# Performance work log

Measured on AMD Instinct MI355X. Metric: run time of the kernel, lower is better.

## Reference

```python
import jax, jax.numpy as jnp
import numpy as np
from jax import lax

GROUPS = 32
EPS = 1e-5
N_STEPS = 8   # fixed-step stand-in for adaptive implicit_adams
N_CORR = 2    # trapezoidal (Adams-Moulton) corrector iterations


def group_norm(x, gamma, beta):
    B, C, H, W = x.shape
    xg = x.reshape(B, GROUPS, C // GROUPS, H, W)
    mean = xg.mean(axis=(2, 3, 4), keepdims=True)
    var = xg.var(axis=(2, 3, 4), keepdims=True)
    xg = (xg - mean) * lax.rsqrt(var + EPS)
    return xg.reshape(B, C, H, W) * gamma[None, :, None, None] + beta[None, :, None, None]


def batch_norm1d(x, gamma, beta):  # training-mode batch stats, x: [B,C,L]
    mean = x.mean(axis=(0, 2), keepdims=True)
    var = x.var(axis=(0, 2), keepdims=True)
    return (x - mean) * lax.rsqrt(var + EPS) * gamma[None, :, None] + beta[None, :, None]


def conv1d(x, w, b):  # x [B,Cin,L], w [Cout,Cin,3], pad=1
    y = lax.conv_general_dilated(x, w, (1,), [(1, 1)], dimension_numbers=('NCH', 'OIH', 'NCH'))
    return y + b[None, :, None]


def concat_conv2d(t, x, w, b):  # x [B,C,H,W], w [C, C+1, 3,3], pad=1
    tt = jnp.full_like(x[:, :1], t)
    ttx = jnp.concatenate([tt, x], axis=1)
    y = lax.conv_general_dilated(ttx, w, (1, 1), [(1, 1), (1, 1)], dimension_numbers=('NCHW', 'OIHW', 'NCHW'))
    return y + b[None, :, None, None]


def make_odefunc(cw1, cb1, gn1_g, gn1_b, gn2_g, gn2_b, cw2, cb2, gn3_g, gn3_b):
    def f(t, x):
        out = jax.nn.relu(group_norm(x, gn1_g, gn1_b))
        out = concat_conv2d(t, out, cw1, cb1)
        out = jax.nn.elu(group_norm(out, gn2_g, gn2_b))
        out = concat_conv2d(t, out, cw2, cb2)
        return group_norm(out, gn3_g, gn3_b)
    return f


def ode_integrate(f, y0):
    h = 1.0 / N_STEPS

    def step(y, i):
        t = i.astype(y.dtype) * h
        f0 = f(t, y)
        y1 = y + h * f0  # explicit predictor
        for _ in range(N_CORR):  # implicit (trapezoidal AM) corrector
            y1 = y + 0.5 * h * (f0 + f(t + h, y1))
        return y1, None

    yT, _ = lax.scan(step, y0, jnp.arange(N_STEPS))
    return yT


def setup_inputs() -> dict:
    key = jax.random.key(0)
    ks = jax.random.split(key, 8)
    B, L, C = 16, 4096, 256
    inp = {
        'x': jax.random.normal(ks[0], (B, 4, 1, L), dtype=jnp.float32),
        'w1': jax.random.normal(ks[1], (64, 4, 3), dtype=jnp.float32) * 0.1,
        'b1': jnp.zeros((64,), jnp.float32),
        'bn1_g': jnp.ones((64,), jnp.float32), 'bn1_b': jnp.zeros((64,), jnp.float32),
        'w2': jax.random.normal(ks[2], (256, 64, 3), dtype=jnp.float32) * 0.05,
        'b2': jnp.zeros((256,), jnp.float32),
        'bn2_g': jnp.ones((256,), jnp.float32), 'bn2_b': jnp.zeros((256,), jnp.float32),
        'cw1': jax.random.normal(ks[3], (C, C + 1, 3, 3), dtype=jnp.float32) * 0.02,
        'cb1': jnp.zeros((C,), jnp.float32),
        'gn1_g': jnp.ones((C,), jnp.float32), 'gn1_b': jnp.zeros((C,), jnp.float32),
        'gn2_g': jnp.ones((C,), jnp.float32), 'gn2_b': jnp.zeros((C,), jnp.float32),
        'cw2': jax.random.normal(ks[4], (C, C + 1, 3, 3), dtype=jnp.float32) * 0.02,
        'cb2': jnp.zeros((C,), jnp.float32),
        'gn3_g': jnp.ones((C,), jnp.float32), 'gn3_b': jnp.zeros((C,), jnp.float32),
    }
    return inp


def reference(x, w1, b1, bn1_g, bn1_b, w2, b2, bn2_g, bn2_b,
              cw1, cb1, gn1_g, gn1_b, gn2_g, gn2_b, cw2, cb2, gn3_g, gn3_b):
    h = x[:, :, 0, :]                       # squeeze(2) -> [B,4,L]
    h = jax.nn.relu(batch_norm1d(conv1d(h, w1, b1), bn1_g, bn1_b))
    h = jnp.tanh(batch_norm1d(conv1d(h, w2, b2), bn2_g, bn2_b))
    y0 = h[:, :, None, :]                   # unsqueeze(2) -> [B,256,1,L]
    f = make_odefunc(cw1, cb1, gn1_g, gn1_b, gn2_g, gn2_b, cw2, cb2, gn3_g, gn3_b)
    return ode_integrate(f, y0)
```

## Files before the change

kernel.cpp:

```cpp
#include <hip/hip_runtime.h>
#include <math.h>

#define L4 4096

typedef short bf16x8 __attribute__((ext_vector_type(8)));
typedef float f32x4 __attribute__((ext_vector_type(4)));

__device__ __forceinline__ unsigned short f2bf(float f) {
  unsigned u = __builtin_bit_cast(unsigned, f);
  return (unsigned short)((u + 0x7FFFu + ((u >> 16) & 1u)) >> 16);
}
__device__ __forceinline__ float bf2f(unsigned short h) {
  unsigned u = ((unsigned)h) << 16;
  return __builtin_bit_cast(float, u);
}
__device__ __forceinline__ unsigned pk2(float lo, float hi) {
  unsigned d;
  asm("v_cvt_pk_bf16_f32 %0, %1, %2" : "=v"(d) : "v"(lo), "v"(hi));
  return d;
}
__device__ __forceinline__ float fast_tanh(float x) {
  float e = __expf(2.f * x);
  return 1.f - 2.f * __builtin_amdgcn_rcpf(e + 1.f);
}

__global__ __launch_bounds__(256) void pack_big(const float* __restrict__ cw,
                                                unsigned short* __restrict__ Apack,
                                                float* __restrict__ Tpack) {
  int gid = blockIdx.x * 256 + threadIdx.x;
  if (gid < 768) {
    int o = gid & 255, tap = gid >> 8;
    Tpack[tap * 256 + o] = cw[((size_t)o * 257) * 9 + 3 + tap];
  }
  if (gid >= 24 * 16 * 64) return;
  int ks = gid >> 10;
  int frow = (gid >> 6) & 15;
  int lane = gid & 63;
  int o = frow * 16 + (lane & 15);
  int tap = ks >> 3;
  int ib = ((ks & 7) << 5) + ((lane >> 4) << 3);
#pragma unroll
  for (int e = 0; e < 8; e++) {
    int i = ib + e;
    Apack[(size_t)gid * 8 + e] = f2bf(cw[((size_t)o * 257 + (i + 1)) * 9 + 3 + tap]);
  }
}

__global__ __launch_bounds__(256) void pack_stem(const float* __restrict__ w2,
                                                 unsigned short* __restrict__ Apack) {
  int gid = blockIdx.x * 256 + threadIdx.x;
  if (gid >= 6 * 16 * 64) return;
  int ks = gid >> 10;
  int frow = (gid >> 6) & 15;
  int lane = gid & 63;
  int o = frow * 16 + (lane & 15);
  int tap = ks >> 1;
  int ib = ((ks & 1) << 5) + ((lane >> 4) << 3);
#pragma unroll
  for (int e = 0; e < 8; e++) {
    int i = ib + e;
    Apack[(size_t)gid * 8 + e] = f2bf(w2[((size_t)o * 64 + i) * 3 + tap]);
  }
}

__global__ __launch_bounds__(256) void conv1_kernel(const float* __restrict__ x,
                                                    const float* __restrict__ w,
                                                    const float* __restrict__ bias,
                                                    unsigned short* __restrict__ out) {
  int idx = blockIdx.x * 256 + threadIdx.x;
  int l = idx & 4095;
  int c = (idx >> 12) & 63;
  int b = idx >> 18;
  const float* xb = x + (size_t)b * 4 * L4;
  const float* wc = w + c * 12;
  float acc = bias[c];
#pragma unroll
  for (int i = 0; i < 4; i++) {
    float x0 = (l > 0) ? xb[i * L4 + l - 1] : 0.f;
    float x1 = xb[i * L4 + l];
    float x2 = (l < 4095) ? xb[i * L4 + l + 1] : 0.f;
    acc += wc[i * 3] * x0 + wc[i * 3 + 1] * x1 + wc[i * 3 + 2] * x2;
  }
  out[idx] = f2bf(acc);
}

__global__ __launch_bounds__(256) void stats_bf16_kernel(const unsigned short* __restrict__ in,
                                                         float* __restrict__ stats,
                                                         int unit_stride, int nrow,
                                                         int row_stride, int rowlen,
                                                         float inv_n) {
  int u = blockIdx.x;
  const unsigned short* base = in + (size_t)u * unit_stride;
  float s = 0.f, s2 = 0.f;
  for (int r = 0; r < nrow; r++) {
    const unsigned short* rowp = base + (size_t)r * row_stride;
    for (int j = threadIdx.x * 4; j < rowlen; j += 256 * 4) {
      ushort4 v = *(const ushort4*)(rowp + j);
      float va = bf2f(v.x), vb = bf2f(v.y), vc = bf2f(v.z), vd = bf2f(v.w);
      s += va + vb + vc + vd;
      s2 += va * va + vb * vb + vc * vc + vd * vd;
    }
  }
  __shared__ float sh[512];
  sh[threadIdx.x] = s;
  sh[256 + threadIdx.x] = s2;
  __syncthreads();
  for (int off = 128; off > 0; off >>= 1) {
    if (threadIdx.x < off) {
      sh[threadIdx.x] += sh[threadIdx.x + off];
      sh[256 + threadIdx.x] += sh[256 + threadIdx.x + off];
    }
    __syncthreads();
  }
  if (threadIdx.x == 0) {
    float m = sh[0] * inv_n;
    float var = sh[256] * inv_n - m * m;
    stats[u * 2] = m;
    stats[u * 2 + 1] = rsqrtf(var + 1e-5f);
  }
}

__global__ __launch_bounds__(256) void act_transpose64(const unsigned short* __restrict__ inv,
                                                       const float* __restrict__ stats,
                                                       const float* __restrict__ gamma,
                                                       const float* __restrict__ beta,
                                                       unsigned short* __restrict__ Xt) {
  constexpr int C = 64;
  __shared__ unsigned short tile[64 * C];
  int bidx = blockIdx.x;
  int b = bidx >> 6;
  int lt = bidx & 63;
  int l0 = lt << 6;
  int t = threadIdx.x;
  int lanel = t & 63;
  int cq = t >> 6;
  for (int cp = 0; cp < C / 4; cp++) {
    int c = cp * 4 + cq;
    float m = stats[2 * c], rs = stats[2 * c + 1];
    float ga = gamma[c] * rs, be = beta[c] - m * ga;
    size_t gidx = ((size_t)b * C + c) * 4096 + l0 + lanel;
    float v = bf2f(inv[gidx]);
    float a = v * ga + be;
    float r = fmaxf(a, 0.f);
    int sw = (lanel & 15) << 2;
    tile[lanel * C + (c ^ sw)] = f2bf(r);
  }
  __syncthreads();
  constexpr int CH = C / 4;
  constexpr int RPP = 256 / CH;
  for (int p = 0; p < 64 / RPP; p++) {
    int r = p * RPP + t / CH;
    int ch = t % CH;
    int sw = (r & 15) << 2;
    ushort4 v = *(const ushort4*)&tile[r * C + ((ch * 4) ^ sw)];
    *(ushort4*)&Xt[((size_t)b * 4098 + 1 + l0 + r) * C + ch * 4] = v;
  }
  if (lt == 0) {
    if (t < C / 4) *(ushort4*)&Xt[((size_t)b * 4098 + 0) * C + t * 4] = make_ushort4(0, 0, 0, 0);
  } else if (lt == 63) {
    if (t < C / 4) *(ushort4*)&Xt[((size_t)b * 4098 + 4097) * C + t * 4] = make_ushort4(0, 0, 0, 0);
  }
}

template <int NKS, int KLG, int CIN, int NORM, int ACT, int NCH, bool INBF, bool TCH, int OUT>
__global__ __launch_bounds__(512, 4) void gemm_T(const void* __restrict__ Bsrc,
                                                 const unsigned short* __restrict__ Apack,
                                                 const float* __restrict__ Pin,
                                                 const float* __restrict__ gng,
                                                 const float* __restrict__ gnb,
                                                 const float* __restrict__ Tpack,
                                                 const float* __restrict__ bias,
                                                 float tval,
                                                 void* __restrict__ outv,
                                                 float* __restrict__ Pout) {
  constexpr int CPR = CIN / 8;
  constexpr int CPRLG = (CIN == 256) ? 5 : 3;
  constexpr int ROWS = 66;
  constexpr int RPI = 512 >> CPRLG;
  constexpr int TOT = ROWS * CPR;
  constexpr int NIT = (TOT + 511) / 512;
  __shared__ unsigned short bsm[ROWS * CIN];
  __shared__ float gsm[32][2];
  __shared__ float ebias[256];
  __shared__ float psh[32][2];

  int tid = threadIdx.x;
  int lane = tid & 63;
  int wv = tid >> 6;
  int b = blockIdx.x >> 6;
  int lt = blockIdx.x & 63;
  int l_base = lt << 6;
  int wo0 = wv << 5;
  int col = lane & 15;
  int grp = lane >> 4;

  int pl = tid & (CPR - 1);
  int row0s = tid >> CPRLG;
  int gch = pl ^ (row0s & 7);
  uint4 hA[NIT];
  uint4 hB[NIT];
#pragma unroll
  for (int it = 0; it < NIT; it++) {
    hA[it] = make_uint4(0, 0, 0, 0);
    if (NORM && !INBF) hB[it] = make_uint4(0, 0, 0, 0);
    int chunk = it * 512 + tid;
    if (chunk < TOT) {
      int row = row0s + it * RPI;
      if (NORM) {
        int gl = l_base - 1 + row;
        if (gl >= 0 && gl < 4096) {
          size_t base = ((size_t)b * 4096 + gl) * CIN + gch * 8;
          if (INBF) {
            hA[it] = *(const uint4*)((const unsigned short*)Bsrc + base);
          } else {
            hA[it] = *(const uint4*)((const float*)Bsrc + base);
            hB[it] = *(const uint4*)((const float*)Bsrc + base + 4);
          }
        }
      } else {
        hA[it] = *(const uint4*)((const unsigned short*)Bsrc +
                                 ((size_t)b * 4098 + l_base + row) * CIN + gch * 8);
      }
    }
  }

  if (NORM) {
    int g = tid >> 4, j0 = tid & 15;
    const float* Pg = Pin + ((size_t)b * 32 + g) * 128;
    float s = 0.f, s2 = 0.f;
    for (int j = j0; j < NCH; j += 16) { s += Pg[j * 2]; s2 += Pg[j * 2 + 1]; }
#pragma unroll
    for (int off = 8; off; off >>= 1) { s += __shfl_down(s, off, 16); s2 += __shfl_down(s2, off, 16); }
    if (j0 == 0) {
      float m = s * (1.f / 32768.f);
      float var = s2 * (1.f / 32768.f) - m * m;
      gsm[g][0] = m;
      gsm[g][1] = rsqrtf(var + 1e-5f);
    }
  }
  if (tid < 256) {
    float e = bias[tid];
    if (TCH) e += tval * (Tpack[tid] + Tpack[256 + tid] + Tpack[512 + tid]);
    ebias[tid] = e;
  }
  if (OUT == 0 && tid >= 256 && tid < 288) { psh[tid - 256][0] = 0.f; psh[tid - 256][1] = 0.f; }
  __syncthreads();

  {
    float ga0 = 1.f, ga1 = 1.f, ga2 = 1.f, ga3 = 1.f, ga4 = 1.f, ga5 = 1.f, ga6 = 1.f, ga7 = 1.f;
    float be0 = 0.f, be1 = 0.f, be2 = 0.f, be3 = 0.f, be4 = 0.f, be5 = 0.f, be6 = 0.f, be7 = 0.f;
    if (NORM) {
      float m = gsm[gch][0], rs = gsm[gch][1];
      float4 g0 = *(const float4*)&gng[gch * 8];
      float4 g1 = *(const float4*)&gng[gch * 8 + 4];
      float4 b0 = *(const float4*)&gnb[gch * 8];
      float4 b1 = *(const float4*)&gnb[gch * 8 + 4];
      ga0 = g0.x * rs; ga1 = g0.y * rs; ga2 = g0.z * rs; ga3 = g0.w * rs;
      ga4 = g1.x * rs; ga5 = g1.y * rs; ga6 = g1.z * rs; ga7 = g1.w * rs;
      be0 = b0.x - m * ga0; be1 = b0.y - m * ga1; be2 = b0.z - m * ga2; be3 = b0.w - m * ga3;
      be4 = b1.x - m * ga4; be5 = b1.y - m * ga5; be6 = b1.z - m * ga6; be7 = b1.w - m * ga7;
    }
#define ACTF(a) ((ACT == 0) ? fmaxf((a), 0.f) : ((a) > 0.f ? (a) : __expf(a) - 1.f))
#pragma unroll
    for (int it = 0; it < NIT; it++) {
      int chunk = it * 512 + tid;
      if (chunk < TOT) {
        int row = row0s + it * RPI;
        uint4 w4;
        if (NORM) {
          int gl = l_base - 1 + row;
          if (gl >= 0 && gl < 4096) {
            float v0, v1, v2, v3, v4, v5, v6, v7;
            if (INBF) {
              v0 = bf2f((unsigned short)(hA[it].x & 0xFFFF)); v1 = bf2f((unsigned short)(hA[it].x >> 16));
              v2 = bf2f((unsigned short)(hA[it].y & 0xFFFF)); v3 = bf2f((unsigned short)(hA[it].y >> 16));
              v4 = bf2f((unsigned short)(hA[it].z & 0xFFFF)); v5 = bf2f((unsigned short)(hA[it].z >> 16));
              v6 = bf2f((unsigned short)(hA[it].w & 0xFFFF)); v7 = bf2f((unsigned short)(hA[it].w >> 16));
            } else {
              v0 = __builtin_bit_cast(float, hA[it].x);
              v1 = __builtin_bit_cast(float, hA[it].y);
              v2 = __builtin_bit_cast(float, hA[it].z);
              v3 = __builtin_bit_cast(float, hA[it].w);
              v4 = __builtin_bit_cast(float, hB[it].x);
              v5 = __builtin_bit_cast(float, hB[it].y);
              v6 = __builtin_bit_cast(float, hB[it].z);
              v7 = __builtin_bit_cast(float, hB[it].w);
            }
            float r0 = ACTF(v0 * ga0 + be0), r1 = ACTF(v1 * ga1 + be1);
            float r2 = ACTF(v2 * ga2 + be2), r3 = ACTF(v3 * ga3 + be3);
            float r4 = ACTF(v4 * ga4 + be4), r5 = ACTF(v5 * ga5 + be5);
            float r6 = ACTF(v6 * ga6 + be6), r7 = ACTF(v7 * ga7 + be7);
            w4.x = pk2(r0, r1); w4.y = pk2(r2, r3);
            w4.z = pk2(r4, r5); w4.w = pk2(r6, r7);
          } else {
            w4 = make_uint4(0, 0, 0, 0);
          }
        } else {
          w4 = hA[it];
        }
        *(uint4*)&bsm[(size_t)chunk * 8] = w4;
      }
    }
#undef ACTF
  }
  __syncthreads();

  const unsigned short* apk = Apack + (size_t)(wv * 2) * 512 + (size_t)lane * 8;

  f32x4 acc[2][4];
#pragma unroll
  for (int i = 0; i < 2; i++)
#pragma unroll
    for (int j = 0; j < 4; j++) acc[i][j] = (f32x4){0.f, 0.f, 0.f, 0.f};

  __builtin_amdgcn_s_setprio(1);
#pragma unroll
  for (int ks = 0; ks < NKS; ks++) {
    int tap = ks >> KLG;
    int cbase = (ks & ((1 << KLG) - 1)) << 2;
    int lr0 = col + tap;
    int cb = (cbase + grp) ^ (lr0 & 7);
    const unsigned short* bp = &bsm[((size_t)(lr0 << CPRLG) + cb) * 8];
    const unsigned short* ap = apk + (size_t)ks * 16 * 512;
    bf16x8 bfr[4], afr[2];
#pragma unroll
    for (int fc = 0; fc < 4; fc++) bfr[fc] = *(const bf16x8*)(bp + fc * 16 * CIN);
#pragma unroll
    for (int fo = 0; fo < 2; fo++) afr[fo] = *(const bf16x8*)(ap + fo * 512);
#pragma unroll
    for (int fo = 0; fo < 2; fo++)
#pragma unroll
      for (int fc = 0; fc < 4; fc++)
        acc[fo][fc] = __builtin_amdgcn_mfma_f32_16x16x32_bf16(afr[fo], bfr[fc], acc[fo][fc], 0, 0, 0);
  }
  __builtin_amdgcn_s_setprio(0);

  float ps = 0.f, ps2 = 0.f;
#pragma unroll
  for (int fo = 0; fo < 2; fo++) {
    int o0 = wo0 + fo * 16 + grp * 4;
    float eb0 = ebias[o0], eb1 = ebias[o0 + 1], eb2 = ebias[o0 + 2], eb3 = ebias[o0 + 3];
    float w0c0 = 0.f, w0c1 = 0.f, w0c2 = 0.f, w0c3 = 0.f;
    float w2c0 = 0.f, w2c1 = 0.f, w2c2 = 0.f, w2c3 = 0.f;
    if (TCH && lt == 0) {
      w0c0 = tval * Tpack[o0]; w0c1 = tval * Tpack[o0 + 1];
      w0c2 = tval * Tpack[o0 + 2]; w0c3 = tval * Tpack[o0 + 3];
    }
    if (TCH && lt == 63) {
      w2c0 = tval * Tpack[512 + o0]; w2c1 = tval * Tpack[512 + o0 + 1];
      w2c2 = tval * Tpack[512 + o0 + 2]; w2c3 = tval * Tpack[512 + o0 + 3];
    }
#pragma unroll
    for (int fc = 0; fc < 4; fc++) {
      int l = l_base + fc * 16 + col;
      float v0 = acc[fo][fc][0] + eb0;
      float v1 = acc[fo][fc][1] + eb1;
      float v2 = acc[fo][fc][2] + eb2;
      float v3 = acc[fo][fc][3] + eb3;
      if (TCH) {
        if (lt == 0 && l == 0) { v0 -= w0c0; v1 -= w0c1; v2 -= w0c2; v3 -= w0c3; }
        if (lt == 63 && l == 4095) { v0 -= w2c0; v1 -= w2c1; v2 -= w2c2; v3 -= w2c3; }
      }
      if (OUT == 0) {
        ps += v0 + v1 + v2 + v3;
        ps2 += v0 * v0 + v1 * v1 + v2 * v2 + v3 * v3;
        uint2 pk = make_uint2(pk2(v0, v1), pk2(v2, v3));
        *(uint2*)((unsigned short*)outv + ((size_t)b * 4096 + l) * 256 + o0) = pk;
      } else if (OUT == 1) {
        float* op = (float*)outv + ((size_t)b * 256 + o0) * 4096 + l;
        op[0] = v0; op[4096] = v1; op[8192] = v2; op[12288] = v3;
      } else {
        unsigned short* op = (unsigned short*)outv + ((size_t)b * 256 + o0) * 4096 + l;
        op[0] = f2bf(v0); op[4096] = f2bf(v1); op[8192] = f2bf(v2); op[12288] = f2bf(v3);
      }
    }
    if (OUT == 0) {
      float s = ps, s2 = ps2;
#pragma unroll
      for (int off = 8; off; off >>= 1) {
        s += __shfl_down(s, off, 16);
        s2 += __shfl_down(s2, off, 16);
      }
      if (col == 0) {
        int g = wv * 4 + fo * 2 + (grp >> 1);
        atomicAdd(&psh[g][0], s);
        atomicAdd(&psh[g][1], s2);
      }
      ps = 0.f; ps2 = 0.f;
    }
  }

  if (OUT == 0) {
    __syncthreads();
    if (tid < 32) {
      size_t pi = ((size_t)b * 32 + tid) * 128 + (size_t)lt * 2;
      Pout[pi] = psh[tid][0];
      Pout[pi + 1] = psh[tid][1];
    }
  }
}

__global__ __launch_bounds__(512) void bn_tanh_T(const unsigned short* __restrict__ Q,
                                                 const float* __restrict__ stats,
                                                 const float* __restrict__ gamma,
                                                 const float* __restrict__ beta,
                                                 unsigned short* __restrict__ Y,
                                                 float* __restrict__ P1) {
  int tid = threadIdx.x;
  int b = blockIdx.x >> 5;
  int seg = blockIdx.x & 31;
  int c = tid >> 1;
  float m = stats[2 * c], rs = stats[2 * c + 1];
  float ga = gamma[c] * rs, be = beta[c] - m * ga;
  __shared__ float psh[32][2];
  if (tid < 32) { psh[tid][0] = 0.f; psh[tid][1] = 0.f; }
  __syncthreads();
  float s = 0.f, s2 = 0.f;
  for (int it = 0; it < 16; it++) {
    int l4 = (tid & 1) + it * 2;
    int l0 = seg * 128 + l4 * 4;
    ushort4 v = *(const ushort4*)&Q[((size_t)b * 256 + c) * 4096 + l0];
    float r0 = fast_tanh(bf2f(v.x) * ga + be);
    float r1 = fast_tanh(bf2f(v.y) * ga + be);
    float r2 = fast_tanh(bf2f(v.z) * ga + be);
    float r3 = fast_tanh(bf2f(v.w) * ga + be);
    Y[((size_t)b * 4096 + l0 + 0) * 256 + c] = f2bf(r0);
    Y[((size_t)b * 4096 + l0 + 1) * 256 + c] = f2bf(r1);
    Y[((size_t)b * 4096 + l0 + 2) * 256 + c] = f2bf(r2);
    Y[((size_t)b * 4096 + l0 + 3) * 256 + c] = f2bf(r3);
    s += r0 + r1 + r2 + r3;
    s2 += r0 * r0 + r1 * r1 + r2 * r2 + r3 * r3;
  }
#pragma unroll
  for (int off = 8; off; off >>= 1) { s += __shfl_down(s, off, 16); s2 += __shfl_down(s2, off, 16); }
  if ((tid & 15) == 0) {
    int g = c >> 3;
    atomicAdd(&psh[g][0], s);
    atomicAdd(&psh[g][1], s2);
  }
  __syncthreads();
  if (tid < 32) {
    size_t pi = ((size_t)b * 32 + tid) * 128 + (size_t)seg * 2;
    P1[pi] = psh[tid][0];
    P1[pi + 1] = psh[tid][1];
  }
}

template <int MODE>
__global__ __launch_bounds__(512) void combine_T(const unsigned short* __restrict__ F,
                                                 const float* __restrict__ P3,
                                                 const float* __restrict__ gng,
                                                 const float* __restrict__ gnb,
                                                 const unsigned short* __restrict__ Yin,
                                                 unsigned short* __restrict__ Out1,
                                                 unsigned short* __restrict__ OutB,
                                                 float* __restrict__ P1) {
  __shared__ float gsm[32][2];
  __shared__ float gabe[256][2];
  __shared__ float psh[32][2];
  int tid = threadIdx.x;
  int b = blockIdx.x >> 5;
  int seg = blockIdx.x & 31;
  {
    int g = tid >> 4, j0 = tid & 15;
    const float* Pg = P3 + ((size_t)b * 32 + g) * 128;
    float s = 0.f, s2 = 0.f;
    for (int j = j0; j < 64; j += 16) { s += Pg[j * 2]; s2 += Pg[j * 2 + 1]; }
#pragma unroll
    for (int off = 8; off; off >>= 1) { s += __shfl_down(s, off, 16); s2 += __shfl_down(s2, off, 16); }
    if (j0 == 0) {
      float m = s * (1.f / 32768.f);
      float var = s2 * (1.f / 32768.f) - m * m;
      gsm[g][0] = m;
      gsm[g][1] = rsqrtf(var + 1e-5f);
    }
  }
  __syncthreads();
  if (tid < 256) {
    float m = gsm[tid >> 3][0], rs = gsm[tid >> 3][1];
    float ga = gng[tid] * rs;
    gabe[tid][0] = ga;
    gabe[tid][1] = gnb[tid] - m * ga;
  }
  if (tid >= 256 && tid < 288) { psh[tid - 256][0] = 0.f; psh[tid - 256][1] = 0.f; }
  __syncthreads();

  size_t base4 = ((size_t)b * 4096 + seg * 128) * 64;
  int c0 = (tid << 2) & 255;
  int g = c0 >> 3;
  float ga0 = gabe[c0][0], be0 = gabe[c0][1];
  float ga1 = gabe[c0 + 1][0], be1 = gabe[c0 + 1][1];
  float ga2 = gabe[c0 + 2][0], be2 = gabe[c0 + 2][1];
  float ga3 = gabe[c0 + 3][0], be3 = gabe[c0 + 3][1];
  float s = 0.f, s2 = 0.f;
  for (int i = tid; i < 8192; i += 512) {
    size_t idx4 = base4 + i;
    ushort4 fv = ((const ushort4*)F)[idx4];
    ushort4 yv = ((const ushort4*)Yin)[idx4];
    float y0 = bf2f(yv.x), y1v = bf2f(yv.y), y2 = bf2f(yv.z), y3 = bf2f(yv.w);
    float f0 = bf2f(fv.x) * ga0 + be0;
    float f1 = bf2f(fv.y) * ga1 + be1;
    float f2 = bf2f(fv.z) * ga2 + be2;
    float f3 = bf2f(fv.w) * ga3 + be3;
    float yn0 = y0 + (MODE == 0 ? 0.125f : 0.0625f) * f0;
    float yn1 = y1v + (MODE == 0 ? 0.125f : 0.0625f) * f1;
    float yn2 = y2 + (MODE == 0 ? 0.125f : 0.0625f) * f2;
    float yn3 = y3 + (MODE == 0 ? 0.125f : 0.0625f) * f3;
    ((uint2*)Out1)[idx4] = make_uint2(pk2(yn0, yn1), pk2(yn2, yn3));
    if (MODE == 0) {
      float yb0 = y0 + 0.0625f * f0;
      float yb1 = y1v + 0.0625f * f1;
      float yb2 = y2 + 0.0625f * f2;
      float yb3 = y3 + 0.0625f * f3;
      ((uint2*)OutB)[idx4] = make_uint2(pk2(yb0, yb1), pk2(yb2, yb3));
    }
    s += yn0 + yn1 + yn2 + yn3;
    s2 += yn0 * yn0 + yn1 * yn1 + yn2 * yn2 + yn3 * yn3;
  }
  s += __shfl_xor(s, 1);
  s2 += __shfl_xor(s2, 1);
  if ((tid & 1) == 0) {
    atomicAdd(&psh[g][0], s);
    atomicAdd(&psh[g][1], s2);
  }
  __syncthreads();
  if (tid < 32) {
    size_t pi = ((size_t)b * 32 + tid) * 128 + (size_t)seg * 2;
    P1[pi] = psh[tid][0];
    P1[pi + 1] = psh[tid][1];
  }
}

__global__ __launch_bounds__(256) void transpose_final(const unsigned short* __restrict__ Y,
                                                       float* __restrict__ out) {
  __shared__ unsigned short tile[64 * 260];
  int b = blockIdx.x >> 6;
  int lt = blockIdx.x & 63;
  int t = threadIdx.x;
  for (int i = t; i < 4096; i += 256) {
    int r = i >> 6;
    int c4 = (i & 63) << 2;
    ushort4 v = *(const ushort4*)&Y[((size_t)b * 4096 + lt * 64 + r) * 256 + c4];
    *(ushort4*)&tile[r * 260 + c4] = v;
  }
  __syncthreads();
  for (int i = t; i < 4096; i += 256) {
    int c = i >> 4;
    int l4 = (i & 15) << 2;
    float4 v;
    v.x = bf2f(tile[(l4 + 0) * 260 + c]);
    v.y = bf2f(tile[(l4 + 1) * 260 + c]);
    v.z = bf2f(tile[(l4 + 2) * 260 + c]);
    v.w = bf2f(tile[(l4 + 3) * 260 + c]);
    *(float4*)&out[((size_t)b * 256 + c) * 4096 + lt * 64 + l4] = v;
  }
}

extern "C" void kernel_launch(void* const* d_in, const int* in_sizes, int n_in,
                              void* d_out, int out_size, void* d_ws, size_t ws_size,
                              hipStream_t stream) {
  const float* x = (const float*)d_in[0];
  const float* w1 = (const float*)d_in[1];
  const float* b1 = (const float*)d_in[2];
  const float* bn1_g = (const float*)d_in[3];
  const float* bn1_b = (const float*)d_in[4];
  const float* w2 = (const float*)d_in[5];
  const float* b2 = (const float*)d_in[6];
  const float* bn2_g = (const float*)d_in[7];
  const float* bn2_b = (const float*)d_in[8];
  const float* cw1 = (const float*)d_in[9];
  const float* cb1 = (const float*)d_in[10];
  const float* gn1_g = (const float*)d_in[11];
  const float* gn1_b = (const float*)d_in[12];
  const float* gn2_g = (const float*)d_in[13];
  const float* gn2_b = (const float*)d_in[14];
  const float* cw2 = (const float*)d_in[15];
  const float* cb2 = (const float*)d_in[16];
  const float* gn3_g = (const float*)d_in[17];
  const float* gn3_b = (const float*)d_in[18];

  const size_t SZ = (size_t)16 * 256 * 4096;

  char* p = (char*)d_ws;
  unsigned short* Ybf = (unsigned short*)p;  p += SZ * 2;
  unsigned short* C1 = (unsigned short*)p;   p += SZ * 2;
  unsigned short* Fb = (unsigned short*)p;   p += SZ * 2;
  unsigned short* APK1 = (unsigned short*)p; p += (size_t)24 * 16 * 64 * 8 * 2;
  unsigned short* APK2 = (unsigned short*)p; p += (size_t)24 * 16 * 64 * 8 * 2;
  unsigned short* APKS = (unsigned short*)p; p += (size_t)6 * 16 * 64 * 8 * 2;
  float* TP1 = (float*)p;                    p += 768 * 4;
  float* TP2 = (float*)p;                    p += 768 * 4;
  float* STATS = (float*)p;                  p += 1024 * 4;
  float* P1 = (float*)p;                     p += (size_t)16 * 32 * 128 * 4;
  float* P2 = (float*)p;                     p += (size_t)16 * 32 * 128 * 4;
  float* P3 = (float*)p;                     p += (size_t)16 * 32 * 128 * 4;

  unsigned short* Qbf = (unsigned short*)d_out;
  unsigned short* Y1 = (unsigned short*)d_out;
  unsigned short* YB = Y1 + SZ;

  pack_big<<<96, 256, 0, stream>>>(cw1, APK1, TP1);
  pack_big<<<96, 256, 0, stream>>>(cw2, APK2, TP2);
  pack_stem<<<24, 256, 0, stream>>>(w2, APKS);

  conv1_kernel<<<16384, 256, 0, stream>>>(x, w1, b1, C1);
  stats_bf16_kernel<<<64, 256, 0, stream>>>(C1, STATS, 4096, 16, 64 * 4096, 4096, 1.f / 65536.f);
  act_transpose64<<<1024, 256, 0, stream>>>(C1, STATS, bn1_g, bn1_b, Fb);
  gemm_T<6, 1, 64, 0, 0, 32, true, false, 2><<<1024, 512, 0, stream>>>(
      Fb, APKS, nullptr, nullptr, nullptr, nullptr, b2, 0.f, Qbf, nullptr);
  stats_bf16_kernel<<<256, 256, 0, stream>>>(Qbf, STATS, 4096, 16, 256 * 4096, 4096, 1.f / 65536.f);
  bn_tanh_T<<<512, 512, 0, stream>>>(Qbf, STATS, bn2_g, bn2_b, Ybf, P1);

  const float H = 0.125f;
  for (int i = 0; i < 8; i++) {
    float t = i * H;
    gemm_T<24, 3, 256, 1, 0, 32, true, true, 0><<<1024, 512, 0, stream>>>(
        Ybf, APK1, P1, gn1_g, gn1_b, TP1, cb1, t, C1, P2);
    gemm_T<24, 3, 256, 1, 1, 64, true, true, 0><<<1024, 512, 0, stream>>>(
        C1, APK2, P2, gn2_g, gn2_b, TP2, cb2, t, Fb, P3);
    combine_T<0><<<512, 512, 0, stream>>>(Fb, P3, gn3_g, gn3_b, Ybf, Y1, YB, P1);
    for (int c = 0; c < 2; c++) {
      gemm_T<24, 3, 256, 1, 0, 32, true, true, 0><<<1024, 512, 0, stream>>>(
          Y1, APK1, P1, gn1_g, gn1_b, TP1, cb1, t + H, C1, P2);
      gemm_T<24, 3, 256, 1, 1, 64, true, true, 0><<<1024, 512, 0, stream>>>(
          C1, APK2, P2, gn2_g, gn2_b, TP2, cb2, t + H, Fb, P3);
      if (c == 0)
        combine_T<1><<<512, 512, 0, stream>>>(Fb, P3, gn3_g, gn3_b, YB, Y1, nullptr, P1);
      else
        combine_T<2><<<512, 512, 0, stream>>>(Fb, P3, gn3_g, gn3_b, YB, Ybf, nullptr, P1);
    }
  }

  transpose_final<<<1024, 256, 0, stream>>>(Ybf, (float*)d_out);
}
```

Before: 2.452 ms.

## Halve gemm block to 256 threads with 64 output channels per wave

The implicit-GEMM conv kernel now runs with 4 waves of 256 threads instead of 8, and each wave computes 64 output channels (4x4 MFMA tiles) instead of 32. This doubles register-level reuse of the B fragments loaded from LDS, so each LDS read of the activation tile feeds twice as many MFMAs. The early register prefetch of the input tile before the GroupNorm statistics reduction is removed; loads now happen inline during the normalize-and-store loop. The trade-offs are higher accumulator register pressure, which can lower occupancy, and less overlap of global loads with the stats computation.

```diff
diff --git a/kernel.cpp b/kernel.cpp
--- a/kernel.cpp
+++ b/kernel.cpp
@@ -163,7 +163,7 @@
 }
 
 template <int NKS, int KLG, int CIN, int NORM, int ACT, int NCH, bool INBF, bool TCH, int OUT>
-__global__ __launch_bounds__(512, 4) void gemm_T(const void* __restrict__ Bsrc,
+__global__ __launch_bounds__(256, 4) void gemm_T(const void* __restrict__ Bsrc,
                                                  const unsigned short* __restrict__ Apack,
                                                  const float* __restrict__ Pin,
                                                  const float* __restrict__ gng,
@@ -176,9 +176,9 @@
   constexpr int CPR = CIN / 8;
   constexpr int CPRLG = (CIN == 256) ? 5 : 3;
   constexpr int ROWS = 66;
-  constexpr int RPI = 512 >> CPRLG;
+  constexpr int RPI = 256 >> CPRLG;
   constexpr int TOT = ROWS * CPR;
-  constexpr int NIT = (TOT + 511) / 512;
+  constexpr int NIT = (TOT + 255) / 256;
   __shared__ unsigned short bsm[ROWS * CIN];
   __shared__ float gsm[32][2];
   __shared__ float ebias[256];
@@ -190,47 +190,17 @@
   int b = blockIdx.x >> 6;
   int lt = blockIdx.x & 63;
   int l_base = lt << 6;
-  int wo0 = wv << 5;
+  int wo0 = wv << 6;
   int col = lane & 15;
   int grp = lane >> 4;
 
-  int pl = tid & (CPR - 1);
-  int row0s = tid >> CPRLG;
-  int gch = pl ^ (row0s & 7);
-  uint4 hA[NIT];
-  uint4 hB[NIT];
-#pragma unroll
-  for (int it = 0; it < NIT; it++) {
-    hA[it] = make_uint4(0, 0, 0, 0);
-    if (NORM && !INBF) hB[it] = make_uint4(0, 0, 0, 0);
-    int chunk = it * 512 + tid;
-    if (chunk < TOT) {
-      int row = row0s + it * RPI;
-      if (NORM) {
-        int gl = l_base - 1 + row;
-        if (gl >= 0 && gl < 4096) {
-          size_t base = ((size_t)b * 4096 + gl) * CIN + gch * 8;
-          if (INBF) {
-            hA[it] = *(const uint4*)((const unsigned short*)Bsrc + base);
-          } else {
-            hA[it] = *(const uint4*)((const float*)Bsrc + base);
-            hB[it] = *(const uint4*)((const float*)Bsrc + base + 4);
-          }
-        }
-      } else {
-        hA[it] = *(const uint4*)((const unsigned short*)Bsrc +
-                                 ((size_t)b * 4098 + l_base + row) * CIN + gch * 8);
-      }
-    }
-  }
-
   if (NORM) {
-    int g = tid >> 4, j0 = tid & 15;
+    int g = tid >> 3, j0 = tid & 7;
     const float* Pg = Pin + ((size_t)b * 32 + g) * 128;
     float s = 0.f, s2 = 0.f;
-    for (int j = j0; j < NCH; j += 16) { s += Pg[j * 2]; s2 += Pg[j * 2 + 1]; }
-#pragma unroll
-    for (int off = 8; off; off >>= 1) { s += __shfl_down(s, off, 16); s2 += __shfl_down(s2, off, 16); }
+    for (int j = j0; j < NCH; j += 8) { s += Pg[j * 2]; s2 += Pg[j * 2 + 1]; }
+#pragma unroll
+    for (int off = 4; off; off >>= 1) { s += __shfl_down(s, off, 8); s2 += __shfl_down(s2, off, 8); }
     if (j0 == 0) {
       float m = s * (1.f / 32768.f);
       float var = s2 * (1.f / 32768.f) - m * m;
@@ -238,15 +208,18 @@
       gsm[g][1] = rsqrtf(var + 1e-5f);
     }
   }
-  if (tid < 256) {
+  {
     float e = bias[tid];
     if (TCH) e += tval * (Tpack[tid] + Tpack[256 + tid] + Tpack[512 + tid]);
     ebias[tid] = e;
   }
-  if (OUT == 0 && tid >= 256 && tid < 288) { psh[tid - 256][0] = 0.f; psh[tid - 256][1] = 0.f; }
+  if (OUT == 0 && tid < 32) { psh[tid][0] = 0.f; psh[tid][1] = 0.f; }
   __syncthreads();
 
   {
+    int pl = tid & (CPR - 1);
+    int row0 = tid >> CPRLG;
+    int gch = pl ^ (row0 & 7);
     float ga0 = 1.f, ga1 = 1.f, ga2 = 1.f, ga3 = 1.f, ga4 = 1.f, ga5 = 1.f, ga6 = 1.f, ga7 = 1.f;
     float be0 = 0.f, be1 = 0.f, be2 = 0.f, be3 = 0.f, be4 = 0.f, be5 = 0.f, be6 = 0.f, be7 = 0.f;
     if (NORM) {
@@ -263,28 +236,26 @@
 #define ACTF(a) ((ACT == 0) ? fmaxf((a), 0.f) : ((a) > 0.f ? (a) : __expf(a) - 1.f))
 #pragma unroll
     for (int it = 0; it < NIT; it++) {
-      int chunk = it * 512 + tid;
+      int chunk = it * 256 + tid;
       if (chunk < TOT) {
-        int row = row0s + it * RPI;
+        int row = row0 + it * RPI;
         uint4 w4;
         if (NORM) {
           int gl = l_base - 1 + row;
           if (gl >= 0 && gl < 4096) {
+            size_t base = ((size_t)b * 4096 + gl) * CIN + gch * 8;
             float v0, v1, v2, v3, v4, v5, v6, v7;
             if (INBF) {
-              v0 = bf2f((unsigned short)(hA[it].x & 0xFFFF)); v1 = bf2f((unsigned short)(hA[it].x >> 16));
-              v2 = bf2f((unsigned short)(hA[it].y & 0xFFFF)); v3 = bf2f((unsigned short)(hA[it].y >> 16));
-              v4 = bf2f((unsigned short)(hA[it].z & 0xFFFF)); v5 = bf2f((unsigned short)(hA[it].z >> 16));
-              v6 = bf2f((unsigned short)(hA[it].w & 0xFFFF)); v7 = bf2f((unsigned short)(hA[it].w >> 16));
+              uint4 raw = *(const uint4*)((const unsigned short*)Bsrc + base);
+              v0 = bf2f((unsigned short)(raw.x & 0xFFFF)); v1 = bf2f((unsigned short)(raw.x >> 16));
+              v2 = bf2f((unsigned short)(raw.y & 0xFFFF)); v3 = bf2f((unsigned short)(raw.y >> 16));
+              v4 = bf2f((unsigned short)(raw.z & 0xFFFF)); v5 = bf2f((unsigned short)(raw.z >> 16));
+              v6 = bf2f((unsigned short)(raw.w & 0xFFFF)); v7 = bf2f((unsigned short)(raw.w >> 16));
             } else {
-              v0 = __builtin_bit_cast(float, hA[it].x);
-              v1 = __builtin_bit_cast(float, hA[it].y);
-              v2 = __builtin_bit_cast(float, hA[it].z);
-              v3 = __builtin_bit_cast(float, hA[it].w);
-              v4 = __builtin_bit_cast(float, hB[it].x);
-              v5 = __builtin_bit_cast(float, hB[it].y);
-              v6 = __builtin_bit_cast(float, hB[it].z);
-              v7 = __builtin_bit_cast(float, hB[it].w);
+              float4 r0 = *(const float4*)((const float*)Bsrc + base);
+              float4 r1 = *(const float4*)((const float*)Bsrc + base + 4);
+              v0 = r0.x; v1 = r0.y; v2 = r0.z; v3 = r0.w;
+              v4 = r1.x; v5 = r1.y; v6 = r1.z; v7 = r1.w;
             }
             float r0 = ACTF(v0 * ga0 + be0), r1 = ACTF(v1 * ga1 + be1);
             float r2 = ACTF(v2 * ga2 + be2), r3 = ACTF(v3 * ga3 + be3);
@@ -296,7 +267,8 @@
             w4 = make_uint4(0, 0, 0, 0);
           }
         } else {
-          w4 = hA[it];
+          w4 = *(const uint4*)((const unsigned short*)Bsrc +
+                               ((size_t)b * 4098 + l_base + row) * CIN + gch * 8);
         }
         *(uint4*)&bsm[(size_t)chunk * 8] = w4;
       }
@@ -305,11 +277,11 @@
   }
   __syncthreads();
 
-  const unsigned short* apk = Apack + (size_t)(wv * 2) * 512 + (size_t)lane * 8;
-
-  f32x4 acc[2][4];
-#pragma unroll
-  for (int i = 0; i < 2; i++)
+  const unsigned short* apk = Apack + (size_t)(wv * 4) * 512 + (size_t)lane * 8;
+
+  f32x4 acc[4][4];
+#pragma unroll
+  for (int i = 0; i < 4; i++)
 #pragma unroll
     for (int j = 0; j < 4; j++) acc[i][j] = (f32x4){0.f, 0.f, 0.f, 0.f};
 
@@ -322,13 +294,13 @@
     int cb = (cbase + grp) ^ (lr0 & 7);
     const unsigned short* bp = &bsm[((size_t)(lr0 << CPRLG) + cb) * 8];
     const unsigned short* ap = apk + (size_t)ks * 16 * 512;
-    bf16x8 bfr[4], afr[2];
+    bf16x8 bfr[4], afr[4];
 #pragma unroll
     for (int fc = 0; fc < 4; fc++) bfr[fc] = *(const bf16x8*)(bp + fc * 16 * CIN);
 #pragma unroll
-    for (int fo = 0; fo < 2; fo++) afr[fo] = *(const bf16x8*)(ap + fo * 512);
-#pragma unroll
-    for (int fo = 0; fo < 2; fo++)
+    for (int fo = 0; fo < 4; fo++) afr[fo] = *(const bf16x8*)(ap + fo * 512);
+#pragma unroll
+    for (int fo = 0; fo < 4; fo++)
 #pragma unroll
       for (int fc = 0; fc < 4; fc++)
         acc[fo][fc] = __builtin_amdgcn_mfma_f32_16x16x32_bf16(afr[fo], bfr[fc], acc[fo][fc], 0, 0, 0);
@@ -337,7 +309,7 @@
 
   float ps = 0.f, ps2 = 0.f;
 #pragma unroll
-  for (int fo = 0; fo < 2; fo++) {
+  for (int fo = 0; fo < 4; fo++) {
     int o0 = wo0 + fo * 16 + grp * 4;
     float eb0 = ebias[o0], eb1 = ebias[o0 + 1], eb2 = ebias[o0 + 2], eb3 = ebias[o0 + 3];
     float w0c0 = 0.f, w0c1 = 0.f, w0c2 = 0.f, w0c3 = 0.f;
@@ -382,7 +354,7 @@
         s2 += __shfl_down(s2, off, 16);
       }
       if (col == 0) {
-        int g = wv * 4 + fo * 2 + (grp >> 1);
+        int g = wv * 8 + fo * 2 + (grp >> 1);
         atomicAdd(&psh[g][0], s);
         atomicAdd(&psh[g][1], s2);
       }
@@ -606,7 +578,7 @@
   conv1_kernel<<<16384, 256, 0, stream>>>(x, w1, b1, C1);
   stats_bf16_kernel<<<64, 256, 0, stream>>>(C1, STATS, 4096, 16, 64 * 4096, 4096, 1.f / 65536.f);
   act_transpose64<<<1024, 256, 0, stream>>>(C1, STATS, bn1_g, bn1_b, Fb);
-  gemm_T<6, 1, 64, 0, 0, 32, true, false, 2><<<1024, 512, 0, stream>>>(
+  gemm_T<6, 1, 64, 0, 0, 32, true, false, 2><<<1024, 256, 0, stream>>>(
       Fb, APKS, nullptr, nullptr, nullptr, nullptr, b2, 0.f, Qbf, nullptr);
   stats_bf16_kernel<<<256, 256, 0, stream>>>(Qbf, STATS, 4096, 16, 256 * 4096, 4096, 1.f / 65536.f);
   bn_tanh_T<<<512, 512, 0, stream>>>(Qbf, STATS, bn2_g, bn2_b, Ybf, P1);
@@ -614,15 +586,15 @@
   const float H = 0.125f;
   for (int i = 0; i < 8; i++) {
     float t = i * H;
-    gemm_T<24, 3, 256, 1, 0, 32, true, true, 0><<<1024, 512, 0, stream>>>(
+    gemm_T<24, 3, 256, 1, 0, 32, true, true, 0><<<1024, 256, 0, stream>>>(
         Ybf, APK1, P1, gn1_g, gn1_b, TP1, cb1, t, C1, P2);
-    gemm_T<24, 3, 256, 1, 1, 64, true, true, 0><<<1024, 512, 0, stream>>>(
+    gemm_T<24, 3, 256, 1, 1, 64, true, true, 0><<<1024, 256, 0, stream>>>(
         C1, APK2, P2, gn2_g, gn2_b, TP2, cb2, t, Fb, P3);
     combine_T<0><<<512, 512, 0, stream>>>(Fb, P3, gn3_g, gn3_b, Ybf, Y1, YB, P1);
     for (int c = 0; c < 2; c++) {
-      gemm_T<24, 3, 256, 1, 0, 32, true, true, 0><<<1024, 512, 0, stream>>>(
+      gemm_T<24, 3, 256, 1, 0, 32, true, true, 0><<<1024, 256, 0, stream>>>(
           Y1, APK1, P1, gn1_g, gn1_b, TP1, cb1, t + H, C1, P2);
-      gemm_T<24, 3, 256, 1, 1, 64, true, true, 0><<<1024, 512, 0, stream>>>(
+      gemm_T<24, 3, 256, 1, 1, 64, true, true, 0><<<1024, 256, 0, stream>>>(
           C1, APK2, P2, gn2_g, gn2_b, TP2, cb2, t + H, Fb, P3);
       if (c == 0)
         combine_T<1><<<512, 512, 0, stream>>>(Fb, P3, gn3_g, gn3_b, YB, Y1, nullptr, P1);
```

Measured after the change: 2.267 ms. -7.6%, faster.
